# Kernel optimization log

Measured on AMD Instinct MI355X. Metric: run time of the kernel, lower is better.

The kernel has to match this reference:

```python
import jax, jax.numpy as jnp
import numpy as np

EPS = 1e-6

def _rmsnorm(x, w):
    # x: [..., Dh]
    inv = jax.lax.rsqrt(jnp.mean(x * x, axis=-1, keepdims=True) + EPS)
    return x * inv * w

def _apply_rope(x, rope):
    # x: [B, H, L, Dh], rope: [L, Dh//2, 2]
    L = x.shape[-2]
    cos = rope[:L, :, 0]  # [L, Dh//2]
    sin = rope[:L, :, 1]
    x_even = x[..., 0::2]
    x_odd = x[..., 1::2]
    rot = jnp.stack([x_even * cos - x_odd * sin,
                     x_even * sin + x_odd * cos], axis=-1)  # [B,H,L,Dh//2,2]
    return rot.reshape(*x.shape[:-1], -1)


def setup_inputs() -> dict:
    key = jax.random.key(0)
    ks = jax.random.split(key, 4)
    B, L, D = 2, 2048, 1024
    H, Dh = 16, 64
    x = jax.random.normal(ks[0], (B, L, D), dtype=jnp.float32)
    rope = jax.random.normal(ks[1], (L, Dh // 2, 2), dtype=jnp.float32)
    w_qkv = jax.random.normal(ks[2], (3 * D, D), dtype=jnp.float32) * (1.0 / np.sqrt(D))
    w_proj = jax.random.normal(ks[3], (D, D), dtype=jnp.float32) * (1.0 / np.sqrt(D))
    q_norm_w = jnp.ones((Dh,), dtype=jnp.float32)
    k_norm_w = jnp.ones((Dh,), dtype=jnp.float32)
    return {"x": x, "rope": rope, "w_qkv": w_qkv, "w_proj": w_proj,
            "q_norm_w": q_norm_w, "k_norm_w": k_norm_w}


def reference(x, rope, w_qkv, w_proj, q_norm_w, k_norm_w):
    B, L, D = x.shape
    H = 16
    Dh = D // H
    qkv = jnp.einsum('bld,ed->ble', x, w_qkv).reshape(B, L, 3, H, Dh)
    qkv = jnp.transpose(qkv, (2, 0, 3, 1, 4))  # [3, B, H, L, Dh]
    q, k, v = qkv[0], qkv[1], qkv[2]
    q = _rmsnorm(q, q_norm_w)
    k = _rmsnorm(k, k_norm_w)
    q = _apply_rope(q, rope)
    k = _apply_rope(k, rope)
    scale = 1.0 / np.sqrt(Dh)
    scores = jnp.einsum('bhqd,bhkd->bhqk', q, k) * scale
    attn = jax.nn.softmax(scores, axis=-1)
    out = jnp.einsum('bhqk,bhkd->bhqd', attn, v)  # [B,H,L,Dh]
    out = jnp.transpose(out, (0, 2, 1, 3)).reshape(B, L, D)
    return jnp.einsum('bld,ed->ble', out, w_proj)
```

## Files before the change

kernel.cpp:

```cpp
#include <hip/hip_runtime.h>

typedef unsigned short u16;
typedef unsigned int u32;
typedef __bf16 bf16x8 __attribute__((ext_vector_type(8)));
typedef float f32x4 __attribute__((ext_vector_type(4)));

#define L_SEQ 2048
#define NH 16
#define DH 64
#define D_MODEL 1024
#define ATT_SHIFT2 14.426950408889634f
#define QSCALE_LOG2E 0.18033688011112042f

__device__ __forceinline__ u16 f2bf(float f) {
  union { float f; u32 u; } v; v.f = f;
  u32 u = v.u;
  return (u16)((u + 0x7fffu + ((u >> 16) & 1u)) >> 16);
}
__device__ __forceinline__ float bf2f(u16 b) {
  union { u32 u; float f; } v; v.u = ((u32)b) << 16;
  return v.f;
}
__device__ __forceinline__ u32 pk2(float lo_val, float hi_val) {
  union { float f; u32 u; } a, b;
  a.f = hi_val; b.f = lo_val;
  return __builtin_amdgcn_perm(a.u + 0x8000u, b.u + 0x8000u, 0x07060302u);
}
__device__ __forceinline__ u32 pk2t(float lo_val, float hi_val) {
  union { float f; u32 u; } a, b;
  a.f = hi_val; b.f = lo_val;
  return __builtin_amdgcn_perm(a.u, b.u, 0x07060302u);
}
__device__ __forceinline__ bf16x8 ld8(const u16* p) {
  union { uint4 u; bf16x8 b; } v;
  v.u = *(const uint4*)p;
  return v.b;
}
__device__ __forceinline__ f32x4 fzero4() { f32x4 z = {0.f, 0.f, 0.f, 0.f}; return z; }

__device__ __forceinline__ float fexp2(float x) {
#if __has_builtin(__builtin_amdgcn_exp2f)
  return __builtin_amdgcn_exp2f(x);
#else
  return __expf(x * 0.6931471805599453f);
#endif
}

__device__ __forceinline__ void gll16(const u16* g, u16* l) {
  __builtin_amdgcn_global_load_lds((const __attribute__((address_space(1))) u32*)g,
                                   (__attribute__((address_space(3))) u32*)l, 16, 0, 0);
}

__global__ __launch_bounds__(256) void cvt_all(const float* __restrict__ x,
                                               const float* __restrict__ wqkv,
                                               const float* __restrict__ wproj,
                                               u16* __restrict__ xb,
                                               u16* __restrict__ wqkvb,
                                               u16* __restrict__ wprojb) {
  int i = blockIdx.x * 256 + threadIdx.x;
  const float* s;
  u16* d;
  int off;
  if (i < 1048576)      { s = x;     d = xb;     off = i; }
  else if (i < 1835008) { s = wqkv;  d = wqkvb;  off = i - 1048576; }
  else                  { s = wproj; d = wprojb; off = i - 1835008; }
  float4 v = ((const float4*)s)[off];
  ((ushort4*)d)[off] = make_ushort4(f2bf(v.x), f2bf(v.y), f2bf(v.z), f2bf(v.w));
}

__global__ __launch_bounds__(256) void gemm_qkv(const u16* __restrict__ A,
                                                const u16* __restrict__ B,
                                                const float* __restrict__ rope,
                                                const float* __restrict__ qw,
                                                const float* __restrict__ kw,
                                                u16* __restrict__ qb,
                                                u16* __restrict__ kb,
                                                u16* __restrict__ vtb) {
  __shared__ u16 smem[16384];
  u16* As = smem;
  u16* Bs = smem + 8192;
  const int t = threadIdx.x;
  const int lane = t & 63, wv = t >> 6;
  const int col = lane & 15, quad = lane >> 4;
  const int wr = wv >> 1, wc = wv & 1;
  const int m0 = blockIdx.y * 128, n0 = blockIdx.x * 128;

  f32x4 acc[4][4];
#pragma unroll
  for (int i = 0; i < 4; ++i)
#pragma unroll
    for (int j = 0; j < 4; ++j) acc[i][j] = fzero4();

  for (int kt = 0; kt < 1024; kt += 64) {
    __syncthreads();
#pragma unroll
    for (int it = 0; it < 4; ++it) {
      int id0 = it * 256 + wv * 64;
      int id = id0 + lane;
      int row = id >> 3, cs = id & 7;
      int csrc = cs ^ (row & 7);
      gll16(A + (size_t)(m0 + row) * 1024 + kt + csrc * 8, As + (size_t)id0 * 8);
      gll16(B + (size_t)(n0 + row) * 1024 + kt + csrc * 8, Bs + (size_t)id0 * 8);
    }
    __syncthreads();
#pragma unroll
    for (int c = 0; c < 2; ++c) {
      bf16x8 af[4], bfv[4];
#pragma unroll
      for (int f = 0; f < 4; ++f) {
        int r = wr * 64 + f * 16 + col;
        af[f] = ld8(&As[(r * 8 + ((c * 4 + quad) ^ (r & 7))) * 8]);
        int rb = wc * 64 + f * 16 + col;
        bfv[f] = ld8(&Bs[(rb * 8 + ((c * 4 + quad) ^ (rb & 7))) * 8]);
      }
#pragma unroll
      for (int i = 0; i < 4; ++i)
#pragma unroll
        for (int j = 0; j < 4; ++j)
          acc[i][j] = __builtin_amdgcn_mfma_f32_16x16x32_bf16(af[i], bfv[j], acc[i][j], 0, 0, 0);
    }
  }

  const int region = n0 >> 10;
  if (region < 2) {
    const float* w = region ? kw : qw;
    u16* dst = region ? kb : qb;
    const float scale = region ? 1.0f : QSCALE_LOG2E;
    const int h = ((n0 & 1023) >> 6) + wc;
    float wloc[4];
#pragma unroll
    for (int j = 0; j < 4; ++j) wloc[j] = w[j * 16 + col];
#pragma unroll
    for (int i = 0; i < 4; ++i) {
#pragma unroll
      for (int r = 0; r < 4; ++r) {
        float v0 = acc[i][0][r], v1 = acc[i][1][r], v2 = acc[i][2][r], v3 = acc[i][3][r];
        float ss = v0 * v0 + v1 * v1 + v2 * v2 + v3 * v3;
        ss += __shfl_xor(ss, 1); ss += __shfl_xor(ss, 2);
        ss += __shfl_xor(ss, 4); ss += __shfl_xor(ss, 8);
        float inv = rsqrtf(ss * (1.f / 64.f) + 1e-6f);
        int gr = m0 + wr * 64 + i * 16 + quad * 4 + r;
        int b = gr >> 11, l = gr & 2047;
        const float2* rope2 = (const float2*)rope + (size_t)l * 32;
        size_t obase = ((size_t)(b * NH + h) * L_SEQ + l) * DH;
        float vv[4] = {v0, v1, v2, v3};
#pragma unroll
        for (int j = 0; j < 4; ++j) {
          float val = vv[j] * inv * wloc[j];
          float part = __shfl_xor(val, 1);
          float2 cs = rope2[j * 8 + (col >> 1)];
          float outv = (lane & 1) ? (part * cs.y + val * cs.x)
                                  : (val * cs.x - part * cs.y);
          dst[obase + j * 16 + col] = f2bf(outv * scale);
        }
      }
    }
  } else {
    __syncthreads();
#pragma unroll
    for (int i = 0; i < 4; ++i) {
      int m_l = wr * 64 + i * 16 + quad * 4;
#pragma unroll
      for (int j = 0; j < 4; ++j) {
        int n_l = wc * 64 + j * 16 + col;
        int ta = n_l * 128 + (m_l ^ ((n_l & 15) << 3));
        *(uint2*)(smem + ta) = make_uint2(pk2(acc[i][j][0], acc[i][j][1]),
                                          pk2(acc[i][j][2], acc[i][j][3]));
      }
    }
    __syncthreads();
    const int b = m0 >> 11, lbase = m0 & 2047;
    const int n_l = t >> 1, mh = (t & 1) * 64;
    const int gc = (n0 - 2048) + n_l;
    const int h = gc >> 6, dh = gc & 63;
    u16* vrow = vtb + ((size_t)(b * NH + h) * DH + dh) * L_SEQ + lbase + mh;
#pragma unroll
    for (int c2 = 0; c2 < 8; ++c2) {
      int m = mh + c2 * 8;
      uint4 v = *(const uint4*)(smem + n_l * 128 + (m ^ ((n_l & 15) << 3)));
      *(uint4*)(vrow + c2 * 8) = v;
    }
  }
}

__global__ __launch_bounds__(256) void attn_flash(const u16* __restrict__ qb,
                                                  const u16* __restrict__ kb,
                                                  const u16* __restrict__ vtb,
                                                  u16* __restrict__ po,
                                                  float* __restrict__ pl) {
  __shared__ u16 ldsK[4096];
  __shared__ u16 ldsV[4096];
  __shared__ u16 ldsP[16384];
  const int t = threadIdx.x;
  const int lane = t & 63, wv = t >> 6;
  const int col = lane & 15, quad = lane >> 4;
  const int bh = blockIdx.x;
  const int half = blockIdx.z;
  const int q0 = blockIdx.y * 256 + wv * 64;

  const u16* kbase = kb + ((size_t)bh * L_SEQ + half * 1024) * DH;
  const u16* vbase = vtb + (size_t)bh * DH * L_SEQ + half * 1024;

  bf16x8 qfrag[4][2];
#pragma unroll
  for (int qf = 0; qf < 4; ++qf)
#pragma unroll
    for (int c = 0; c < 2; ++c)
      qfrag[qf][c] = ld8(qb + ((size_t)bh * L_SEQ + q0 + qf * 16 + col) * DH + c * 32 + quad * 8);

  f32x4 o[4][4];
#pragma unroll
  for (int qf = 0; qf < 4; ++qf)
#pragma unroll
    for (int nf = 0; nf < 4; ++nf) o[qf][nf] = fzero4();
  float lrow[4] = {0.f, 0.f, 0.f, 0.f};

  u16* pb = &ldsP[wv * 4096];
  const int kc_w = (quad >> 1);
  const int sub = (quad & 1) * 4;

  for (int tt = 0; tt < 16; ++tt) {
    __syncthreads();
    {
      const int kt = tt * 64;
#pragma unroll
      for (int it = 0; it < 2; ++it) {
        int id0 = it * 256 + wv * 64;
        int id = id0 + lane;
        int row = id >> 3, cs = id & 7, csrc = cs ^ (row & 7);
        gll16(kbase + (size_t)(kt + row) * DH + csrc * 8, ldsK + (size_t)id0 * 8);
        gll16(vbase + (size_t)row * L_SEQ + kt + csrc * 8, ldsV + (size_t)id0 * 8);
      }
    }
    __syncthreads();

#pragma unroll
    for (int mf = 0; mf < 4; ++mf) {
      const int kr = mf * 16 + col;
      bf16x8 kf0 = ld8(&ldsK[kr * 64 + (((0 + quad) ^ (kr & 7)) * 8)]);
      bf16x8 kf1 = ld8(&ldsK[kr * 64 + (((4 + quad) ^ (kr & 7)) * 8)]);
      f32x4 s[4];
#pragma unroll
      for (int qf = 0; qf < 4; ++qf) {
        s[qf] = __builtin_amdgcn_mfma_f32_16x16x32_bf16(kf0, qfrag[qf][0], fzero4(), 0, 0, 0);
        s[qf] = __builtin_amdgcn_mfma_f32_16x16x32_bf16(kf1, qfrag[qf][1], s[qf], 0, 0, 0);
      }
      const int kc = mf * 2 + kc_w;
#pragma unroll
      for (int qf = 0; qf < 4; ++qf) {
        float e0 = fexp2(s[qf][0] - ATT_SHIFT2);
        float e1 = fexp2(s[qf][1] - ATT_SHIFT2);
        float e2 = fexp2(s[qf][2] - ATT_SHIFT2);
        float e3 = fexp2(s[qf][3] - ATT_SHIFT2);
        lrow[qf] += (e0 + e1) + (e2 + e3);
        const int q = qf * 16 + col;
        const int slot = q * 8 + (kc ^ (q & 7));
        *(uint2*)(pb + slot * 8 + sub) = make_uint2(pk2t(e0, e1), pk2t(e2, e3));
      }
    }

#pragma unroll
    for (int c = 0; c < 2; ++c) {
      bf16x8 pa[4];
#pragma unroll
      for (int qf = 0; qf < 4; ++qf) {
        const int q = qf * 16 + col;
        pa[qf] = ld8(pb + (q * 8 + ((c * 4 + quad) ^ (q & 7))) * 8);
      }
#pragma unroll
      for (int nf = 0; nf < 4; ++nf) {
        int vr = nf * 16 + col;
        bf16x8 vf = ld8(&ldsV[vr * 64 + (((c * 4 + quad) ^ (vr & 7)) * 8)]);
#pragma unroll
        for (int qf = 0; qf < 4; ++qf)
          o[qf][nf] = __builtin_amdgcn_mfma_f32_16x16x32_bf16(pa[qf], vf, o[qf][nf], 0, 0, 0);
      }
    }
  }

  u16* pob = po + (size_t)(half * 32 + bh) * L_SEQ * DH;
#pragma unroll
  for (int qf = 0; qf < 4; ++qf) {
    lrow[qf] += __shfl_xor(lrow[qf], 16);
    lrow[qf] += __shfl_xor(lrow[qf], 32);
    if (quad == 0)
      pl[(size_t)(half * 32 + bh) * L_SEQ + q0 + qf * 16 + col] = lrow[qf];
#pragma unroll
    for (int nf = 0; nf < 4; ++nf)
#pragma unroll
      for (int r = 0; r < 4; ++r)
        pob[(size_t)(q0 + qf * 16 + quad * 4 + r) * DH + nf * 16 + col] = f2bf(o[qf][nf][r]);
  }
}

__global__ __launch_bounds__(256) void gemm2_cmb(const u16* __restrict__ po,
                                                 const float* __restrict__ pl,
                                                 const u16* __restrict__ B,
                                                 float* __restrict__ out) {
  __shared__ u16 As[64 * 64];
  __shared__ u16 Bs[128 * 64];
  const int t = threadIdx.x;
  const int lane = t & 63, wv = t >> 6;
  const int col = lane & 15, quad = lane >> 4;
  const int wr = wv >> 1, wc = wv & 1;
  const int m0 = blockIdx.y * 64, n0 = blockIdx.x * 128;
  const int srow = t >> 2, kc0 = (t & 3) * 2;
  const int m = m0 + srow, bb = m >> 11, ll = m & 2047;

  f32x4 acc[2][4];
#pragma unroll
  for (int i = 0; i < 2; ++i)
#pragma unroll
    for (int j = 0; j < 4; ++j) acc[i][j] = fzero4();

  for (int kt = 0; kt < 1024; kt += 64) {
    __syncthreads();
    {
      int h = kt >> 6;
      size_t lidx = (size_t)(bb * 16 + h) * L_SEQ + ll;
      float inv = 1.0f / (pl[lidx] + pl[65536 + lidx]);
      size_t rowoff = lidx * 64;
#pragma unroll
      for (int i = 0; i < 2; ++i) {
        int kc = kc0 + i;
        uint4 a0 = *(const uint4*)(po + rowoff + kc * 8);
        uint4 a1 = *(const uint4*)(po + 4194304 + rowoff + kc * 8);
        union { uint4 u; u16 s[8]; } ua, ub;
        ua.u = a0; ub.u = a1;
        float r[8];
#pragma unroll
        for (int j = 0; j < 8; ++j) r[j] = (bf2f(ua.s[j]) + bf2f(ub.s[j])) * inv;
        uint4 pk = make_uint4(pk2(r[0], r[1]), pk2(r[2], r[3]), pk2(r[4], r[5]), pk2(r[6], r[7]));
        int slot = srow * 8 + (kc ^ (srow & 7));
        *(uint4*)(As + slot * 8) = pk;
      }
    }
#pragma unroll
    for (int it = 0; it < 4; ++it) {
      int id0 = it * 256 + wv * 64;
      int id = id0 + lane;
      int row = id >> 3, cs = id & 7, csrc = cs ^ (row & 7);
      gll16(B + (size_t)(n0 + row) * 1024 + kt + csrc * 8, Bs + (size_t)id0 * 8);
    }
    __syncthreads();
#pragma unroll
    for (int c = 0; c < 2; ++c) {
      bf16x8 af[2], bfv[4];
#pragma unroll
      for (int f = 0; f < 2; ++f) {
        int r = wr * 32 + f * 16 + col;
        af[f] = ld8(&As[(r * 8 + ((c * 4 + quad) ^ (r & 7))) * 8]);
      }
#pragma unroll
      for (int f = 0; f < 4; ++f) {
        int rb = wc * 64 + f * 16 + col;
        bfv[f] = ld8(&Bs[(rb * 8 + ((c * 4 + quad) ^ (rb & 7))) * 8]);
      }
#pragma unroll
      for (int i = 0; i < 2; ++i)
#pragma unroll
        for (int j = 0; j < 4; ++j)
          acc[i][j] = __builtin_amdgcn_mfma_f32_16x16x32_bf16(af[i], bfv[j], acc[i][j], 0, 0, 0);
    }
  }
#pragma unroll
  for (int i = 0; i < 2; ++i) {
    int gr = m0 + wr * 32 + i * 16 + quad * 4;
#pragma unroll
    for (int j = 0; j < 4; ++j) {
      int gc = n0 + wc * 64 + j * 16 + col;
#pragma unroll
      for (int r = 0; r < 4; ++r)
        out[(size_t)(gr + r) * D_MODEL + gc] = acc[i][j][r];
    }
  }
}

extern "C" void kernel_launch(void* const* d_in, const int* in_sizes, int n_in,
                              void* d_out, int out_size, void* d_ws, size_t ws_size,
                              hipStream_t stream) {
  const float* x     = (const float*)d_in[0];
  const float* rope  = (const float*)d_in[1];
  const float* wqkv  = (const float*)d_in[2];
  const float* wproj = (const float*)d_in[3];
  const float* qnw   = (const float*)d_in[4];
  const float* knw   = (const float*)d_in[5];
  float* out = (float*)d_out;
  char* ws = (char*)d_ws;

  u16* xb     = (u16*)(ws + 0);
  u16* wqkvb  = (u16*)(ws + 8388608);
  u16* wprojb = (u16*)(ws + 14680064);
  u16* qb     = (u16*)(ws + 16777216);
  u16* kb     = (u16*)(ws + 25165824);
  u16* vtb    = (u16*)(ws + 33554432);
  u16* po     = (u16*)(ws + 41943040);
  float* pl   = (float*)(ws + 58720256);

  cvt_all<<<8192, 256, 0, stream>>>(x, wqkv, wproj, xb, wqkvb, wprojb);

  gemm_qkv<<<dim3(24, 32), 256, 0, stream>>>(xb, wqkvb, rope, qnw, knw, qb, kb, vtb);

  attn_flash<<<dim3(32, 8, 2), 256, 0, stream>>>(qb, kb, vtb, po, pl);

  gemm2_cmb<<<dim3(8, 64), 256, 0, stream>>>(po, pl, wprojb, out);
}
```

Before: 208.0 us.

## Load K/V fragments directly into registers in attention, drop LDS staging and barriers

The attention kernel stops staging K and V tiles through shared memory with two barriers per tile. Each wave now loads its K and V MFMA fragments straight from global memory into registers, and prefetches the next K tile before the PV product. The grid is flattened to 1D so the two key-halves of one head sit in adjacent blocks, and launch bounds request 2 blocks per CU. The aim is to remove barrier stalls and LDS traffic, at the cost of redundant global and L2 reads across the four waves and higher register pressure.

```diff
diff --git a/kernel.cpp b/kernel.cpp
--- a/kernel.cpp
+++ b/kernel.cpp
@@ -183,20 +183,19 @@
   }
 }
 
-__global__ __launch_bounds__(256) void attn_flash(const u16* __restrict__ qb,
-                                                  const u16* __restrict__ kb,
-                                                  const u16* __restrict__ vtb,
-                                                  u16* __restrict__ po,
-                                                  float* __restrict__ pl) {
-  __shared__ u16 ldsK[4096];
-  __shared__ u16 ldsV[4096];
+__global__ __launch_bounds__(256, 2) void attn_flash(const u16* __restrict__ qb,
+                                                     const u16* __restrict__ kb,
+                                                     const u16* __restrict__ vtb,
+                                                     u16* __restrict__ po,
+                                                     float* __restrict__ pl) {
   __shared__ u16 ldsP[16384];
   const int t = threadIdx.x;
   const int lane = t & 63, wv = t >> 6;
   const int col = lane & 15, quad = lane >> 4;
-  const int bh = blockIdx.x;
-  const int half = blockIdx.z;
-  const int q0 = blockIdx.y * 256 + wv * 64;
+  const int bhh = blockIdx.x & 63;
+  const int bh = bhh >> 1;
+  const int half = bhh & 1;
+  const int q0 = (blockIdx.x >> 6) * 256 + wv * 64;
 
   const u16* kbase = kb + ((size_t)bh * L_SEQ + half * 1024) * DH;
   const u16* vbase = vtb + (size_t)bh * DH * L_SEQ + half * 1024;
@@ -219,31 +218,28 @@
   const int kc_w = (quad >> 1);
   const int sub = (quad & 1) * 4;
 
+  bf16x8 kreg[8], vreg[8];
+#pragma unroll
+  for (int mf = 0; mf < 4; ++mf)
+#pragma unroll
+    for (int c = 0; c < 2; ++c)
+      kreg[mf * 2 + c] = ld8(kbase + (size_t)(mf * 16 + col) * DH + c * 32 + quad * 8);
+
   for (int tt = 0; tt < 16; ++tt) {
-    __syncthreads();
-    {
-      const int kt = tt * 64;
-#pragma unroll
-      for (int it = 0; it < 2; ++it) {
-        int id0 = it * 256 + wv * 64;
-        int id = id0 + lane;
-        int row = id >> 3, cs = id & 7, csrc = cs ^ (row & 7);
-        gll16(kbase + (size_t)(kt + row) * DH + csrc * 8, ldsK + (size_t)id0 * 8);
-        gll16(vbase + (size_t)row * L_SEQ + kt + csrc * 8, ldsV + (size_t)id0 * 8);
-      }
-    }
-    __syncthreads();
+    const int kt = tt * 64;
+#pragma unroll
+    for (int nf = 0; nf < 4; ++nf)
+#pragma unroll
+      for (int c = 0; c < 2; ++c)
+        vreg[nf * 2 + c] = ld8(vbase + (size_t)(nf * 16 + col) * L_SEQ + kt + c * 32 + quad * 8);
 
 #pragma unroll
     for (int mf = 0; mf < 4; ++mf) {
-      const int kr = mf * 16 + col;
-      bf16x8 kf0 = ld8(&ldsK[kr * 64 + (((0 + quad) ^ (kr & 7)) * 8)]);
-      bf16x8 kf1 = ld8(&ldsK[kr * 64 + (((4 + quad) ^ (kr & 7)) * 8)]);
       f32x4 s[4];
 #pragma unroll
       for (int qf = 0; qf < 4; ++qf) {
-        s[qf] = __builtin_amdgcn_mfma_f32_16x16x32_bf16(kf0, qfrag[qf][0], fzero4(), 0, 0, 0);
-        s[qf] = __builtin_amdgcn_mfma_f32_16x16x32_bf16(kf1, qfrag[qf][1], s[qf], 0, 0, 0);
+        s[qf] = __builtin_amdgcn_mfma_f32_16x16x32_bf16(kreg[mf * 2 + 0], qfrag[qf][0], fzero4(), 0, 0, 0);
+        s[qf] = __builtin_amdgcn_mfma_f32_16x16x32_bf16(kreg[mf * 2 + 1], qfrag[qf][1], s[qf], 0, 0, 0);
       }
       const int kc = mf * 2 + kc_w;
 #pragma unroll
@@ -259,6 +255,15 @@
       }
     }
 
+    if (tt < 15) {
+      const int kn = kt + 64;
+#pragma unroll
+      for (int mf = 0; mf < 4; ++mf)
+#pragma unroll
+        for (int c = 0; c < 2; ++c)
+          kreg[mf * 2 + c] = ld8(kbase + (size_t)(kn + mf * 16 + col) * DH + c * 32 + quad * 8);
+    }
+
 #pragma unroll
     for (int c = 0; c < 2; ++c) {
       bf16x8 pa[4];
@@ -268,13 +273,10 @@
         pa[qf] = ld8(pb + (q * 8 + ((c * 4 + quad) ^ (q & 7))) * 8);
       }
 #pragma unroll
-      for (int nf = 0; nf < 4; ++nf) {
-        int vr = nf * 16 + col;
-        bf16x8 vf = ld8(&ldsV[vr * 64 + (((c * 4 + quad) ^ (vr & 7)) * 8)]);
+      for (int nf = 0; nf < 4; ++nf)
 #pragma unroll
         for (int qf = 0; qf < 4; ++qf)
-          o[qf][nf] = __builtin_amdgcn_mfma_f32_16x16x32_bf16(pa[qf], vf, o[qf][nf], 0, 0, 0);
-      }
+          o[qf][nf] = __builtin_amdgcn_mfma_f32_16x16x32_bf16(pa[qf], vreg[nf * 2 + c], o[qf][nf], 0, 0, 0);
     }
   }
 
@@ -401,7 +403,7 @@
 
   gemm_qkv<<<dim3(24, 32), 256, 0, stream>>>(xb, wqkvb, rope, qnw, knw, qb, kb, vtb);
 
-  attn_flash<<<dim3(32, 8, 2), 256, 0, stream>>>(qb, kb, vtb, po, pl);
+  attn_flash<<<512, 256, 0, stream>>>(qb, kb, vtb, po, pl);
 
   gemm2_cmb<<<dim3(8, 64), 256, 0, stream>>>(po, pl, wprojb, out);
 }
```

Result: slower. 222.1 us (+6.8%).

## Split attention keys four ways, compute row sums via MFMA, use DPP reductions

Applied to the files above, without the earlier changes.

The attention kernel now splits the key range into four partitions instead of two, which doubles the grid to 1024 blocks for better occupancy and latency hiding. The projection kernel now combines four partial outputs and four partial sums, which costs more global reads. Row sums of the exponentials are produced by an extra MFMA against a vector of ones instead of scalar adds and shuffles. The fixed softmax shift is removed. In the QKV epilogue, xor-shuffles are replaced with DPP moves, and the workspace is re-laid out so the bf16 x and weight buffers alias the po buffer. Dropping the shift risks overflow in the bf16 exponentials, and the buffer aliasing depends on launch order.

```diff
diff --git a/kernel.cpp b/kernel.cpp
--- a/kernel.cpp
+++ b/kernel.cpp
@@ -9,7 +9,6 @@
 #define NH 16
 #define DH 64
 #define D_MODEL 1024
-#define ATT_SHIFT2 14.426950408889634f
 #define QSCALE_LOG2E 0.18033688011112042f
 
 __device__ __forceinline__ u16 f2bf(float f) {
@@ -44,6 +43,12 @@
 #else
   return __expf(x * 0.6931471805599453f);
 #endif
+}
+
+template <int CTRL>
+__device__ __forceinline__ float dpp_mov(float x) {
+  return __int_as_float(__builtin_amdgcn_update_dpp(
+      0, __float_as_int(x), CTRL, 0xf, 0xf, true));
 }
 
 __device__ __forceinline__ void gll16(const u16* g, u16* l) {
@@ -136,8 +141,10 @@
       for (int r = 0; r < 4; ++r) {
         float v0 = acc[i][0][r], v1 = acc[i][1][r], v2 = acc[i][2][r], v3 = acc[i][3][r];
         float ss = v0 * v0 + v1 * v1 + v2 * v2 + v3 * v3;
-        ss += __shfl_xor(ss, 1); ss += __shfl_xor(ss, 2);
-        ss += __shfl_xor(ss, 4); ss += __shfl_xor(ss, 8);
+        ss += dpp_mov<0x121>(ss);
+        ss += dpp_mov<0x122>(ss);
+        ss += dpp_mov<0x124>(ss);
+        ss += dpp_mov<0x128>(ss);
         float inv = rsqrtf(ss * (1.f / 64.f) + 1e-6f);
         int gr = m0 + wr * 64 + i * 16 + quad * 4 + r;
         int b = gr >> 11, l = gr & 2047;
@@ -147,7 +154,7 @@
 #pragma unroll
         for (int j = 0; j < 4; ++j) {
           float val = vv[j] * inv * wloc[j];
-          float part = __shfl_xor(val, 1);
+          float part = dpp_mov<0xB1>(val);
           float2 cs = rope2[j * 8 + (col >> 1)];
           float outv = (lane & 1) ? (part * cs.y + val * cs.x)
                                   : (val * cs.x - part * cs.y);
@@ -195,11 +202,11 @@
   const int lane = t & 63, wv = t >> 6;
   const int col = lane & 15, quad = lane >> 4;
   const int bh = blockIdx.x;
-  const int half = blockIdx.z;
+  const int qtr = blockIdx.z;
   const int q0 = blockIdx.y * 256 + wv * 64;
 
-  const u16* kbase = kb + ((size_t)bh * L_SEQ + half * 1024) * DH;
-  const u16* vbase = vtb + (size_t)bh * DH * L_SEQ + half * 1024;
+  const u16* kbase = kb + ((size_t)bh * L_SEQ + qtr * 512) * DH;
+  const u16* vbase = vtb + (size_t)bh * DH * L_SEQ + qtr * 512;
 
   bf16x8 qfrag[4][2];
 #pragma unroll
@@ -208,18 +215,23 @@
     for (int c = 0; c < 2; ++c)
       qfrag[qf][c] = ld8(qb + ((size_t)bh * L_SEQ + q0 + qf * 16 + col) * DH + c * 32 + quad * 8);
 
-  f32x4 o[4][4];
-#pragma unroll
-  for (int qf = 0; qf < 4; ++qf)
+  bf16x8 ones;
+#pragma unroll
+  for (int j = 0; j < 8; ++j) ones[j] = (__bf16)1.0f;
+
+  f32x4 o[4][4], ol[4];
+#pragma unroll
+  for (int qf = 0; qf < 4; ++qf) {
 #pragma unroll
     for (int nf = 0; nf < 4; ++nf) o[qf][nf] = fzero4();
-  float lrow[4] = {0.f, 0.f, 0.f, 0.f};
+    ol[qf] = fzero4();
+  }
 
   u16* pb = &ldsP[wv * 4096];
   const int kc_w = (quad >> 1);
   const int sub = (quad & 1) * 4;
 
-  for (int tt = 0; tt < 16; ++tt) {
+  for (int tt = 0; tt < 8; ++tt) {
     __syncthreads();
     {
       const int kt = tt * 64;
@@ -248,11 +260,10 @@
       const int kc = mf * 2 + kc_w;
 #pragma unroll
       for (int qf = 0; qf < 4; ++qf) {
-        float e0 = fexp2(s[qf][0] - ATT_SHIFT2);
-        float e1 = fexp2(s[qf][1] - ATT_SHIFT2);
-        float e2 = fexp2(s[qf][2] - ATT_SHIFT2);
-        float e3 = fexp2(s[qf][3] - ATT_SHIFT2);
-        lrow[qf] += (e0 + e1) + (e2 + e3);
+        float e0 = fexp2(s[qf][0]);
+        float e1 = fexp2(s[qf][1]);
+        float e2 = fexp2(s[qf][2]);
+        float e3 = fexp2(s[qf][3]);
         const int q = qf * 16 + col;
         const int slot = q * 8 + (kc ^ (q & 7));
         *(uint2*)(pb + slot * 8 + sub) = make_uint2(pk2t(e0, e1), pk2t(e2, e3));
@@ -275,16 +286,20 @@
         for (int qf = 0; qf < 4; ++qf)
           o[qf][nf] = __builtin_amdgcn_mfma_f32_16x16x32_bf16(pa[qf], vf, o[qf][nf], 0, 0, 0);
       }
-    }
-  }
-
-  u16* pob = po + (size_t)(half * 32 + bh) * L_SEQ * DH;
+#pragma unroll
+      for (int qf = 0; qf < 4; ++qf)
+        ol[qf] = __builtin_amdgcn_mfma_f32_16x16x32_bf16(pa[qf], ones, ol[qf], 0, 0, 0);
+    }
+  }
+
+  u16* pob = po + (size_t)(qtr * 32 + bh) * L_SEQ * DH;
+  float* plb = pl + (size_t)(qtr * 32 + bh) * L_SEQ + q0;
 #pragma unroll
   for (int qf = 0; qf < 4; ++qf) {
-    lrow[qf] += __shfl_xor(lrow[qf], 16);
-    lrow[qf] += __shfl_xor(lrow[qf], 32);
-    if (quad == 0)
-      pl[(size_t)(half * 32 + bh) * L_SEQ + q0 + qf * 16 + col] = lrow[qf];
+    if (col == 0) {
+#pragma unroll
+      for (int r = 0; r < 4; ++r) plb[qf * 16 + quad * 4 + r] = ol[qf][r];
+    }
 #pragma unroll
     for (int nf = 0; nf < 4; ++nf)
 #pragma unroll
@@ -318,18 +333,22 @@
     {
       int h = kt >> 6;
       size_t lidx = (size_t)(bb * 16 + h) * L_SEQ + ll;
-      float inv = 1.0f / (pl[lidx] + pl[65536 + lidx]);
+      float lsum = pl[lidx] + pl[65536 + lidx] + pl[131072 + lidx] + pl[196608 + lidx];
+      float inv = 1.0f / lsum;
       size_t rowoff = lidx * 64;
 #pragma unroll
       for (int i = 0; i < 2; ++i) {
         int kc = kc0 + i;
         uint4 a0 = *(const uint4*)(po + rowoff + kc * 8);
         uint4 a1 = *(const uint4*)(po + 4194304 + rowoff + kc * 8);
-        union { uint4 u; u16 s[8]; } ua, ub;
-        ua.u = a0; ub.u = a1;
+        uint4 a2 = *(const uint4*)(po + 8388608 + rowoff + kc * 8);
+        uint4 a3 = *(const uint4*)(po + 12582912 + rowoff + kc * 8);
+        union { uint4 u; u16 s[8]; } u0, u1, u2, u3;
+        u0.u = a0; u1.u = a1; u2.u = a2; u3.u = a3;
         float r[8];
 #pragma unroll
-        for (int j = 0; j < 8; ++j) r[j] = (bf2f(ua.s[j]) + bf2f(ub.s[j])) * inv;
+        for (int j = 0; j < 8; ++j)
+          r[j] = (bf2f(u0.s[j]) + bf2f(u1.s[j]) + bf2f(u2.s[j]) + bf2f(u3.s[j])) * inv;
         uint4 pk = make_uint4(pk2(r[0], r[1]), pk2(r[2], r[3]), pk2(r[4], r[5]), pk2(r[6], r[7]));
         int slot = srow * 8 + (kc ^ (srow & 7));
         *(uint4*)(As + slot * 8) = pk;
@@ -388,20 +407,20 @@
   float* out = (float*)d_out;
   char* ws = (char*)d_ws;
 
-  u16* xb     = (u16*)(ws + 0);
-  u16* wqkvb  = (u16*)(ws + 8388608);
-  u16* wprojb = (u16*)(ws + 14680064);
-  u16* qb     = (u16*)(ws + 16777216);
-  u16* kb     = (u16*)(ws + 25165824);
-  u16* vtb    = (u16*)(ws + 33554432);
-  u16* po     = (u16*)(ws + 41943040);
-  float* pl   = (float*)(ws + 58720256);
+  u16* qb     = (u16*)(ws + 0);
+  u16* kb     = (u16*)(ws + 8388608);
+  u16* vtb    = (u16*)(ws + 16777216);
+  u16* wprojb = (u16*)(ws + 25165824);
+  u16* po     = (u16*)(ws + 27262976);
+  float* pl   = (float*)(ws + 60817408);
+  u16* xb     = (u16*)(ws + 27262976);
+  u16* wqkvb  = (u16*)(ws + 35651584);
 
   cvt_all<<<8192, 256, 0, stream>>>(x, wqkv, wproj, xb, wqkvb, wprojb);
 
   gemm_qkv<<<dim3(24, 32), 256, 0, stream>>>(xb, wqkvb, rope, qnw, knw, qb, kb, vtb);
 
-  attn_flash<<<dim3(32, 8, 2), 256, 0, stream>>>(qb, kb, vtb, po, pl);
+  attn_flash<<<dim3(32, 8, 4), 256, 0, stream>>>(qb, kb, vtb, po, pl);
 
   gemm2_cmb<<<dim3(8, 64), 256, 0, stream>>>(po, pl, wprojb, out);
 }
```

Measured after the change: 237.8 us. 1.14x slower.
